# Kernel optimization log

Hardware: AMD Instinct MI355X
Metric: run time of the kernel (lower is better)

Reference implementation:

```python
import jax, jax.numpy as jnp
import numpy as np

B, D_IN, H = 128, 256, 256


def setup_inputs() -> dict:
    key = jax.random.key(0)
    ks = jax.random.split(key, 16)
    d = {}
    d["x_t"] = jax.random.normal(ks[0], (B, D_IN), jnp.float32)
    d["h_c1"] = jax.random.normal(ks[1], (B, H), jnp.float32)
    d["h_c2"] = jax.random.normal(ks[2], (B, H), jnp.float32)
    for i in range(4):
        d[f"gm{i}"] = jax.random.normal(ks[3 + i], (B, H), jnp.float32) * 0.1
    for i in range(4, 8):
        d[f"gm{i}"] = jax.random.normal(ks[3 + i], (B, D_IN, H), jnp.float32) * 0.1
    # exp-exp parameterization: r = exp(-exp(r_param)) with r ~ U(0,1)
    u_r = jax.random.uniform(ks[11], (1, H), jnp.float32, 0.01, 0.99)
    d["r_param"] = jnp.log(-jnp.log(u_r))
    # theta = exp(theta_param) with theta ~ U(0, pi)
    u_t = jax.random.uniform(ks[12], (1, H), jnp.float32, 0.01, float(np.pi))
    d["theta_param"] = jnp.log(u_t)
    scale = 1.0 / np.sqrt(D_IN)
    d["wx1"] = jax.random.normal(ks[13], (D_IN, H), jnp.float32) * scale
    d["wx2"] = jax.random.normal(ks[14], (D_IN, H), jnp.float32) * scale
    return d


def reference(x_t, h_c1, h_c2, gm0, gm1, gm2, gm3, gm4, gm5, gm6, gm7,
              r_param, theta_param, wx1, wx2):
    h_c1 = jax.lax.stop_gradient(h_c1)
    h_c2 = jax.lax.stop_gradient(h_c2)

    # exp-exp parameterization of the complex pole g + i*phi
    exp_r = jnp.exp(r_param)          # (1, H)
    r = jnp.exp(-exp_r)               # |pole| in (0, 1)
    theta = jnp.exp(theta_param)      # pole angle
    g = r * jnp.cos(theta)
    phi = r * jnp.sin(theta)
    norm = jnp.sqrt(1.0 - r * r)      # input normalization

    w1x = x_t @ wx1                   # (B, H)
    w2x = x_t @ wx2

    c1 = g * h_c1 - phi * h_c2 + norm * w1x
    c2 = g * h_c2 + phi * h_c1 + norm * w2x

    h1_post = jax.nn.relu(c1)
    h2_post = jax.nn.relu(c2)
    d1 = (c1 > 0).astype(c1.dtype)
    d2 = (c2 > 0).astype(c2.dtype)

    # derivatives of (g, phi, norm) wrt r_param / theta_param
    d_g_w_r = -exp_r * g
    d_phi_w_r = -exp_r * phi
    d_g_w_th = -theta * phi
    d_phi_w_th = theta * g
    d_norm_w_r = exp_r * (r * r) / norm

    # eligibility traces for r_param / theta_param: (B, H)
    ngm0 = d1 * (d_g_w_r * h_c1 + g * gm0 - d_phi_w_r * h_c2 - phi * gm1 + d_norm_w_r * w1x)
    ngm1 = d2 * (d_g_w_r * h_c2 + g * gm1 + d_phi_w_r * h_c1 + phi * gm0 + d_norm_w_r * w2x)
    ngm2 = d1 * (d_g_w_th * h_c1 + g * gm2 - d_phi_w_th * h_c2 - phi * gm3)
    ngm3 = d2 * (d_g_w_th * h_c2 + g * gm3 + d_phi_w_th * h_c1 + phi * gm2)

    # eligibility traces for input weights: (B, D_in, H); outer product x_t ⊗ norm
    x_outer = x_t[:, :, None]         # (B, D, 1) broadcasts against (1, H)
    d1e = d1[:, None, :]
    d2e = d2[:, None, :]
    ngm4 = d1e * (g * gm4 - phi * gm5 + norm * x_outer)  # c1 wrt wx1
    ngm5 = d2e * (g * gm5 + phi * gm4)                   # c2 wrt wx1
    ngm6 = d1e * (g * gm6 - phi * gm7)                   # c1 wrt wx2
    ngm7 = d2e * (g * gm7 + phi * gm6 + norm * x_outer)  # c2 wrt wx2

    new_gm = tuple(jax.lax.stop_gradient(t) for t in (ngm0, ngm1, ngm2, ngm3, ngm4, ngm5, ngm6, ngm7))
    return (h1_post, h2_post) + new_gm
```

## Files before the change

### kernel.cpp

```cpp
#include <hip/hip_runtime.h>

#define B    128
#define D_IN 256
#define H    256

#define BH      (B * H)
#define BIG     (B * D_IN * H)
#define OFF_H1   0
#define OFF_H2   (1 * BH)
#define OFF_NGM0 (2 * BH)
#define OFF_NGM1 (3 * BH)
#define OFF_NGM2 (4 * BH)
#define OFF_NGM3 (5 * BH)
#define OFF_NGM4 (6 * BH)
#define OFF_NGM5 (OFF_NGM4 + 1 * BIG)
#define OFF_NGM6 (OFF_NGM4 + 2 * BIG)
#define OFF_NGM7 (OFF_NGM4 + 3 * BIG)

typedef float floatx4 __attribute__((ext_vector_type(4)));

__global__ __launch_bounds__(256, 2) void k_small(
    const float* __restrict__ x,   const float* __restrict__ hc1, const float* __restrict__ hc2,
    const float* __restrict__ gm0, const float* __restrict__ gm1,
    const float* __restrict__ gm2, const float* __restrict__ gm3,
    const float* __restrict__ rp,  const float* __restrict__ thp,
    const float* __restrict__ wx1, const float* __restrict__ wx2,
    float* __restrict__ out, float* __restrict__ ws)
{
    const int bid  = blockIdx.x;
    const int b    = bid >> 2;
    const int hseg = bid & 3;
    const int t    = threadIdx.x;

    __shared__ float  xs[D_IN];
    __shared__ float4 s1q[16 * 16];
    __shared__ float4 s2q[16 * 16];

    xs[t] = x[b * D_IN + t];
    __syncthreads();

    const int hq = t & 15;
    const int ks = t >> 4;
    const int gq = hseg * 16 + hq;

    const float4* __restrict__ wx1q = (const float4*)wx1;
    const float4* __restrict__ wx2q = (const float4*)wx2;

    float4 a1 = make_float4(0.f, 0.f, 0.f, 0.f);
    float4 a2 = make_float4(0.f, 0.f, 0.f, 0.f);
    const int k0 = ks * 16;
#pragma unroll
    for (int kk = 0; kk < 16; ++kk) {
        const int k = k0 + kk;
        const float xv = xs[k];
        const float4 w1 = wx1q[k * 64 + gq];
        const float4 w2 = wx2q[k * 64 + gq];
        a1.x = fmaf(xv, w1.x, a1.x); a1.y = fmaf(xv, w1.y, a1.y);
        a1.z = fmaf(xv, w1.z, a1.z); a1.w = fmaf(xv, w1.w, a1.w);
        a2.x = fmaf(xv, w2.x, a2.x); a2.y = fmaf(xv, w2.y, a2.y);
        a2.z = fmaf(xv, w2.z, a2.z); a2.w = fmaf(xv, w2.w, a2.w);
    }
    s1q[ks * 16 + hq] = a1;
    s2q[ks * 16 + hq] = a2;
    __syncthreads();

    if (t < 64) {
        const int h   = hseg * 64 + t;
        const float* s1f = (const float*)s1q;
        const float* s2f = (const float*)s2q;
        float acc1 = 0.f, acc2 = 0.f;
#pragma unroll
        for (int s = 0; s < 16; ++s) {
            acc1 += s1f[s * 64 + t];
            acc2 += s2f[s * 64 + t];
        }

        const float er  = expf(rp[h]);
        const float r   = expf(-er);
        const float th  = expf(thp[h]);
        const float g   = r * cosf(th);
        const float phi = r * sinf(th);
        const float nrm = sqrtf(1.0f - r * r);

        const int idx = b * H + h;
        const float h1 = hc1[idx], h2 = hc2[idx];

        const float c1 = g * h1 - phi * h2 + nrm * acc1;
        const float c2 = g * h2 + phi * h1 + nrm * acc2;
        const float d1 = (c1 > 0.0f) ? 1.0f : 0.0f;
        const float d2 = (c2 > 0.0f) ? 1.0f : 0.0f;

        out[OFF_H1 + idx] = fmaxf(c1, 0.0f);
        out[OFF_H2 + idx] = fmaxf(c2, 0.0f);

        const float m0 = gm0[idx], m1 = gm1[idx], m2 = gm2[idx], m3 = gm3[idx];

        const float dgr = -er * g;
        const float dpr = -er * phi;
        const float dgt = -th * phi;
        const float dpt =  th * g;
        const float dnr =  er * r * r / nrm;

        out[OFF_NGM0 + idx] = d1 * (dgr * h1 + g * m0 - dpr * h2 - phi * m1 + dnr * acc1);
        out[OFF_NGM1 + idx] = d2 * (dgr * h2 + g * m1 + dpr * h1 + phi * m0 + dnr * acc2);
        out[OFF_NGM2 + idx] = d1 * (dgt * h1 + g * m2 - dpt * h2 - phi * m3);
        out[OFF_NGM3 + idx] = d2 * (dgt * h2 + g * m3 + dpt * h1 + phi * m2);

        ws[0 * BH + idx] = d1 * g;
        ws[1 * BH + idx] = d1 * phi;
        ws[2 * BH + idx] = d1 * nrm;
        ws[3 * BH + idx] = d2 * g;
        ws[4 * BH + idx] = d2 * phi;
        ws[5 * BH + idx] = d2 * nrm;
    }
}

__global__ __launch_bounds__(256) void k_big(
    const float4* __restrict__ gm4, const float4* __restrict__ gm5,
    const float4* __restrict__ gm6, const float4* __restrict__ gm7,
    const float*  __restrict__ x,
    const float4* __restrict__ wsq,
    floatx4* __restrict__ o4, floatx4* __restrict__ o5,
    floatx4* __restrict__ o6, floatx4* __restrict__ o7)
{
    const int i  = blockIdx.x * 256 + threadIdx.x;
    const int b  = i >> 14;
    const int j  = (i >> 6) & (D_IN - 1);
    const int h4 = i & 63;

    const int CQ = BH / 4;
    const int ci = (b << 6) + h4;

    const float4 A1 = wsq[0 * CQ + ci];
    const float4 B1 = wsq[1 * CQ + ci];
    const float4 N1 = wsq[2 * CQ + ci];
    const float4 A2 = wsq[3 * CQ + ci];
    const float4 B2 = wsq[4 * CQ + ci];
    const float4 N2 = wsq[5 * CQ + ci];

    const float xv = x[(b << 8) + j];

    const float4 g4 = gm4[i], g5 = gm5[i], g6 = gm6[i], g7 = gm7[i];

    floatx4 r4, r5, r6, r7;
#define COMP(c, n)                                                    \
    r4[n] = fmaf(N1.c, xv, fmaf(A1.c, g4.c, -(B1.c * g5.c)));         \
    r5[n] = fmaf(A2.c, g5.c, B2.c * g4.c);                            \
    r6[n] = fmaf(A1.c, g6.c, -(B1.c * g7.c));                         \
    r7[n] = fmaf(N2.c, xv, fmaf(A2.c, g7.c, B2.c * g6.c));
    COMP(x, 0) COMP(y, 1) COMP(z, 2) COMP(w, 3)
#undef COMP

    __builtin_nontemporal_store(r4, &o4[i]);
    __builtin_nontemporal_store(r5, &o5[i]);
    __builtin_nontemporal_store(r6, &o6[i]);
    __builtin_nontemporal_store(r7, &o7[i]);
}

extern "C" void kernel_launch(void* const* d_in, const int* in_sizes, int n_in,
                              void* d_out, int out_size, void* d_ws, size_t ws_size,
                              hipStream_t stream) {
    const float* x_t  = (const float*)d_in[0];
    const float* hc1  = (const float*)d_in[1];
    const float* hc2  = (const float*)d_in[2];
    const float* gm0  = (const float*)d_in[3];
    const float* gm1  = (const float*)d_in[4];
    const float* gm2  = (const float*)d_in[5];
    const float* gm3  = (const float*)d_in[6];
    const float* gm4  = (const float*)d_in[7];
    const float* gm5  = (const float*)d_in[8];
    const float* gm6  = (const float*)d_in[9];
    const float* gm7  = (const float*)d_in[10];
    const float* rp   = (const float*)d_in[11];
    const float* thp  = (const float*)d_in[12];
    const float* wx1  = (const float*)d_in[13];
    const float* wx2  = (const float*)d_in[14];

    float* out = (float*)d_out;
    float* ws  = (float*)d_ws;

    k_small<<<B * 4, 256, 0, stream>>>(x_t, hc1, hc2, gm0, gm1, gm2, gm3,
                                       rp, thp, wx1, wx2, out, ws);

    const int quads = BIG / 4;
    k_big<<<quads / 256, 256, 0, stream>>>(
        (const float4*)gm4, (const float4*)gm5, (const float4*)gm6, (const float4*)gm7,
        x_t, (const float4*)ws,
        (floatx4*)(out + OFF_NGM4), (floatx4*)(out + OFF_NGM5),
        (floatx4*)(out + OFF_NGM6), (floatx4*)(out + OFF_NGM7));
}
```

Before: 271.6 us.

## Split big eligibility kernel into paired halves with two quads per thread

The big elementwise kernel now runs as two groups of blocks: one handles the gm4/gm5 pair and the other the gm6/gm7 pair. Each thread processes two float4 quads 256 apart, and the input streams are read with nontemporal loads. The aim is fewer live input streams per block, more memory requests in flight per thread, and less cache pollution on this bandwidth-bound 268 MB read/write pass. In exchange, the per-block workspace and x loads are duplicated across the two groups, and occupancy is now pinned through launch bounds.

```diff
diff --git a/kernel.cpp b/kernel.cpp
--- a/kernel.cpp
+++ b/kernel.cpp
@@ -115,46 +115,61 @@
     }
 }
 
-__global__ __launch_bounds__(256) void k_big(
-    const float4* __restrict__ gm4, const float4* __restrict__ gm5,
-    const float4* __restrict__ gm6, const float4* __restrict__ gm7,
+__global__ __launch_bounds__(256, 4) void k_big(
+    const floatx4* __restrict__ gm4, const floatx4* __restrict__ gm5,
+    const floatx4* __restrict__ gm6, const floatx4* __restrict__ gm7,
     const float*  __restrict__ x,
-    const float4* __restrict__ wsq,
+    const floatx4* __restrict__ wsq,
     floatx4* __restrict__ o4, floatx4* __restrict__ o5,
     floatx4* __restrict__ o6, floatx4* __restrict__ o7)
 {
-    const int i  = blockIdx.x * 256 + threadIdx.x;
-    const int b  = i >> 14;
-    const int j  = (i >> 6) & (D_IN - 1);
-    const int h4 = i & 63;
-
-    const int CQ = BH / 4;
-    const int ci = (b << 6) + h4;
-
-    const float4 A1 = wsq[0 * CQ + ci];
-    const float4 B1 = wsq[1 * CQ + ci];
-    const float4 N1 = wsq[2 * CQ + ci];
-    const float4 A2 = wsq[3 * CQ + ci];
-    const float4 B2 = wsq[4 * CQ + ci];
-    const float4 N2 = wsq[5 * CQ + ci];
-
-    const float xv = x[(b << 8) + j];
-
-    const float4 g4 = gm4[i], g5 = gm5[i], g6 = gm6[i], g7 = gm7[i];
-
-    floatx4 r4, r5, r6, r7;
-#define COMP(c, n)                                                    \
-    r4[n] = fmaf(N1.c, xv, fmaf(A1.c, g4.c, -(B1.c * g5.c)));         \
-    r5[n] = fmaf(A2.c, g5.c, B2.c * g4.c);                            \
-    r6[n] = fmaf(A1.c, g6.c, -(B1.c * g7.c));                         \
-    r7[n] = fmaf(N2.c, xv, fmaf(A2.c, g7.c, B2.c * g6.c));
-    COMP(x, 0) COMP(y, 1) COMP(z, 2) COMP(w, 3)
-#undef COMP
-
-    __builtin_nontemporal_store(r4, &o4[i]);
-    __builtin_nontemporal_store(r5, &o5[i]);
-    __builtin_nontemporal_store(r6, &o6[i]);
-    __builtin_nontemporal_store(r7, &o7[i]);
+    const int g    = blockIdx.x >> 12;
+    const int bid2 = blockIdx.x & 4095;
+    const int q_lo = bid2 * 512 + threadIdx.x;
+    const int q_hi = q_lo + 256;
+
+    const int b   = q_lo >> 14;
+    const int j   = (q_lo >> 6) & (D_IN - 1);
+    const int h4  = q_lo & 63;
+    const int CQ  = BH / 4;
+    const int ci  = (b << 6) + h4;
+
+    const floatx4* __restrict__ pa = g ? gm6 : gm4;
+    const floatx4* __restrict__ pb = g ? gm7 : gm5;
+    floatx4* __restrict__ oa = g ? o6 : o4;
+    floatx4* __restrict__ ob = g ? o7 : o5;
+
+    const floatx4 A1 = wsq[0 * CQ + ci];
+    const floatx4 B1 = wsq[1 * CQ + ci];
+    const floatx4 A2 = wsq[3 * CQ + ci];
+    const floatx4 B2 = wsq[4 * CQ + ci];
+    const floatx4 NN = wsq[(g ? 5 : 2) * CQ + ci];
+
+    const float x_lo = x[(b << 8) + j];
+    const float x_hi = x[(b << 8) + j + 4];
+    const float fxa_lo = g ? 0.f : x_lo;
+    const float fxa_hi = g ? 0.f : x_hi;
+    const float fxb_lo = g ? x_lo : 0.f;
+    const float fxb_hi = g ? x_hi : 0.f;
+
+    const floatx4 a_lo = __builtin_nontemporal_load(&pa[q_lo]);
+    const floatx4 b_lo = __builtin_nontemporal_load(&pb[q_lo]);
+    const floatx4 a_hi = __builtin_nontemporal_load(&pa[q_hi]);
+    const floatx4 b_hi = __builtin_nontemporal_load(&pb[q_hi]);
+
+    floatx4 ra_lo, rb_lo, ra_hi, rb_hi;
+#pragma unroll
+    for (int n = 0; n < 4; ++n) {
+        ra_lo[n] = fmaf(NN[n], fxa_lo, fmaf(A1[n], a_lo[n], -(B1[n] * b_lo[n])));
+        rb_lo[n] = fmaf(NN[n], fxb_lo, fmaf(A2[n], b_lo[n],   B2[n] * a_lo[n]));
+        ra_hi[n] = fmaf(NN[n], fxa_hi, fmaf(A1[n], a_hi[n], -(B1[n] * b_hi[n])));
+        rb_hi[n] = fmaf(NN[n], fxb_hi, fmaf(A2[n], b_hi[n],   B2[n] * a_hi[n]));
+    }
+
+    __builtin_nontemporal_store(ra_lo, &oa[q_lo]);
+    __builtin_nontemporal_store(rb_lo, &ob[q_lo]);
+    __builtin_nontemporal_store(ra_hi, &oa[q_hi]);
+    __builtin_nontemporal_store(rb_hi, &ob[q_hi]);
 }
 
 extern "C" void kernel_launch(void* const* d_in, const int* in_sizes, int n_in,
@@ -182,10 +197,9 @@
     k_small<<<B * 4, 256, 0, stream>>>(x_t, hc1, hc2, gm0, gm1, gm2, gm3,
                                        rp, thp, wx1, wx2, out, ws);
 
-    const int quads = BIG / 4;
-    k_big<<<quads / 256, 256, 0, stream>>>(
-        (const float4*)gm4, (const float4*)gm5, (const float4*)gm6, (const float4*)gm7,
-        x_t, (const float4*)ws,
+    k_big<<<8192, 256, 0, stream>>>(
+        (const floatx4*)gm4, (const floatx4*)gm5, (const floatx4*)gm6, (const floatx4*)gm7,
+        x_t, (const floatx4*)ws,
         (floatx4*)(out + OFF_NGM4), (floatx4*)(out + OFF_NGM5),
         (floatx4*)(out + OFF_NGM6), (floatx4*)(out + OFF_NGM7));
 }
```

Result: faster. 257.1 us (-5.4%).
